# Optimization experiments

Hardware: AMD Instinct MI355X
Metric: run time of the kernel (lower is better)

The kernel has to match this reference:

```python
import jax, jax.numpy as jnp
import numpy as np

DIM = 96
GROUPS = 8          # SPPE factor
CG = DIM // GROUPS  # channels per SPPE group = 12
D_STATE = 16
D_CONV = 4
D_INNER = 2 * DIM   # expand=2
DT_RANK = 6         # ceil(96/16)
EPS = 1e-5


def setup_inputs() -> dict:
    key = jax.random.key(0)
    ks = jax.random.split(key, 16)
    def w(k, shape, s=0.02):
        return (jax.random.normal(k, shape) * s).astype(jnp.float32)
    z = lambda *s: jnp.zeros(s, jnp.float32)
    inp = {
        "x": jax.random.normal(ks[0], (2, DIM, 32, 32, 32), dtype=jnp.float32),
        # SPPE params
        "sppe_c1_w": w(ks[1], (CG, CG)), "sppe_c1_b": z(CG),
        "sppe_c3_w": w(ks[2], (CG, CG, 3, 3, 3)), "sppe_c3_b": z(CG),
        "sppe_gn_w": jnp.ones((CG,), jnp.float32), "sppe_gn_b": z(CG),
        # Mamba params (mamba_ssm defaults: proj biases False, conv bias True)
        "in_proj_w": w(ks[3], (2 * D_INNER, DIM)),
        "conv1d_w": w(ks[4], (D_INNER, D_CONV), 0.1), "conv1d_b": z(D_INNER),
        "x_proj_w": w(ks[5], (DT_RANK + 2 * D_STATE, D_INNER)),
        "dt_proj_w": w(ks[6], (D_INNER, DT_RANK), 0.1),
        "dt_proj_b": w(ks[7], (D_INNER,), 0.1),
        "A_log": jnp.log(jnp.tile(jnp.arange(1, D_STATE + 1, dtype=jnp.float32), (D_INNER, 1))),
        "ssm_D": jnp.ones((D_INNER,), jnp.float32),
        "out_proj_w": w(ks[8], (DIM, D_INNER)),
        # MlpChannel params (1x1 Conv3d == pointwise linear over channels)
        "mlp_fc1_w": w(ks[9], (4 * DIM, DIM)), "mlp_fc1_b": z(4 * DIM),
        "mlp_fc2_w": w(ks[10], (DIM, 4 * DIM)), "mlp_fc2_b": z(DIM),
    }
    return inp


def _inorm(x):
    # InstanceNorm3d (affine=False, biased var) over spatial dims per (b,c)
    m = jnp.mean(x, axis=(2, 3, 4), keepdims=True)
    v = jnp.var(x, axis=(2, 3, 4), keepdims=True)
    return (x - m) * jax.lax.rsqrt(v + EPS)


def _sppe(x, c1_w, c1_b, c3_w, c3_b, gn_w, gn_b):
    b, c, h, w, d = x.shape
    bg = b * GROUPS
    gx = x.reshape(bg, CG, h, w, d)
    # directional pools, each ending as (bg, CG, axis_len, 1, 1)
    x_h = jnp.mean(gx, axis=(3, 4), keepdims=True)                      # (bg,CG,h,1,1)
    x_w = jnp.mean(gx, axis=(2, 4), keepdims=True).transpose(0, 1, 3, 2, 4)
    x_d = jnp.mean(gx, axis=(2, 3), keepdims=True).transpose(0, 1, 4, 3, 2)
    hwd = jnp.concatenate([x_h, x_w, x_d], axis=2)[..., 0, 0]          # (bg,CG,h+w+d)
    hwd = jnp.einsum("oc,bcn->bon", c1_w, hwd) + c1_b[:, None]
    g_h = jax.nn.sigmoid(hwd[:, :, :h])[:, :, :, None, None]           # (bg,CG,h,1,1)
    g_w = jax.nn.sigmoid(hwd[:, :, h:h + w])[:, :, None, :, None]      # (bg,CG,1,w,1)
    g_d = jax.nn.sigmoid(hwd[:, :, h + w:])[:, :, None, None, :]       # (bg,CG,1,1,d)
    gated = gx * g_h * g_w * g_d
    # GroupNorm(num_groups=CG, num_channels=CG) == per-channel norm + affine
    gm = jnp.mean(gated, axis=(2, 3, 4), keepdims=True)
    gv = jnp.var(gated, axis=(2, 3, 4), keepdims=True)
    x1 = (gated - gm) * jax.lax.rsqrt(gv + EPS)
    x1 = x1 * gn_w[:, None, None, None] + gn_b[:, None, None, None]
    x2 = jax.lax.conv_general_dilated(
        gx, c3_w, (1, 1, 1), [(1, 1)] * 3,
        dimension_numbers=("NCDHW", "OIDHW", "NCDHW")) + c3_b[:, None, None, None]
    n = h * w * d
    x11 = jax.nn.softmax(jnp.mean(x1, axis=(2, 3, 4)), axis=-1)        # (bg,CG)
    x21 = jax.nn.softmax(jnp.mean(x2, axis=(2, 3, 4)), axis=-1)
    x12 = x2.reshape(bg, CG, n)
    x22 = x1.reshape(bg, CG, n)
    weights = (jnp.einsum("bc,bcn->bn", x11, x12)
               + jnp.einsum("bc,bcn->bn", x21, x22)).reshape(bg, 1, h, w, d)
    return (gx * jax.nn.sigmoid(weights)).reshape(b, c, h, w, d)


def _mamba(seq, in_proj_w, conv1d_w, conv1d_b, x_proj_w, dt_proj_w, dt_proj_b,
           A_log, ssm_D, out_proj_w):
    # seq: (B, L, DIM)
    B, L, _ = seq.shape
    xz = seq @ in_proj_w.T                       # (B,L,2*E)
    xm, zg = jnp.split(xz, 2, axis=-1)
    # depthwise causal conv1d along L
    xc = jax.lax.conv_general_dilated(
        xm.transpose(0, 2, 1), conv1d_w[:, None, :], (1,), [(D_CONV - 1, 0)],
        dimension_numbers=("NCH", "OIH", "NCH"), feature_group_count=D_INNER)
    xc = jax.nn.silu((xc + conv1d_b[:, None]).transpose(0, 2, 1))  # (B,L,E)
    dbl = xc @ x_proj_w.T                         # (B,L,DT_RANK+2N)
    dt = jax.nn.softplus(dbl[..., :DT_RANK] @ dt_proj_w.T + dt_proj_b)  # (B,L,E)
    Bm = dbl[..., DT_RANK:DT_RANK + D_STATE]      # (B,L,N)
    Cm = dbl[..., DT_RANK + D_STATE:]             # (B,L,N)
    A = -jnp.exp(A_log)                           # (E,N)

    def step(h, t):
        dt_t, b_t, c_t, x_t = t                   # (B,E),(B,N),(B,N),(B,E)
        dA = jnp.exp(dt_t[:, :, None] * A)        # (B,E,N)
        h = h * dA + (dt_t * x_t)[:, :, None] * b_t[:, None, :]
        return h, jnp.einsum("ben,bn->be", h, c_t)

    h0 = jnp.zeros((B, D_INNER, D_STATE), seq.dtype)
    _, ys = jax.lax.scan(step, h0, (dt.transpose(1, 0, 2), Bm.transpose(1, 0, 2),
                                    Cm.transpose(1, 0, 2), xc.transpose(1, 0, 2)))
    y = ys.transpose(1, 0, 2) + xc * ssm_D
    y = y * jax.nn.silu(zg)
    return y @ out_proj_w.T                       # (B,L,DIM)


def reference(x, sppe_c1_w, sppe_c1_b, sppe_c3_w, sppe_c3_b, sppe_gn_w, sppe_gn_b,
              in_proj_w, conv1d_w, conv1d_b, x_proj_w, dt_proj_w, dt_proj_b,
              A_log, ssm_D, out_proj_w, mlp_fc1_w, mlp_fc1_b, mlp_fc2_w, mlp_fc2_b):
    y_sppe = _sppe(x, sppe_c1_w, sppe_c1_b, sppe_c3_w, sppe_c3_b, sppe_gn_w, sppe_gn_b)
    B, C, H, W, Dd = x.shape
    L = H * W * Dd
    seq = _inorm(x).reshape(B, C, L).transpose(0, 2, 1)           # (B,L,C)
    out = _mamba(seq, in_proj_w, conv1d_w, conv1d_b, x_proj_w,
                 dt_proj_w, dt_proj_b, A_log, ssm_D, out_proj_w)
    xo = out.transpose(0, 2, 1).reshape(B, C, H, W, Dd)
    xo = _inorm(xo) * y_sppe
    t = jnp.einsum("oc,bchwd->bohwd", mlp_fc1_w, xo) + mlp_fc1_b[:, None, None, None]
    t = jax.nn.gelu(t, approximate=False)
    t = jnp.einsum("oc,bchwd->bohwd", mlp_fc2_w, t) + mlp_fc2_b[:, None, None, None]
    return t + x
```

## Files before the change

kernel.cpp:

```cpp
#include <hip/hip_runtime.h>
#include <math.h>

#define NSPA 32768
#define TCH 32
#define NCH 1024
#define EPS 1e-5f

#define ST_MEAN   0
#define ST_RSTD   192
#define ST_GM     384
#define ST_GRSTD  576
#define ST_X2SUM  768
#define ST_XH     1024
#define ST_XW     7168
#define ST_XD     13312
#define ST_GATE   19456
#define ST_MEAN2  38400
#define ST_RSTD2  38592
#define ST_WT     40960

__device__ __forceinline__ float sigmoidf_(float x){ return 1.f/(1.f+__expf(-x)); }
__device__ __forceinline__ float siluf_(float x){ return x/(1.f+__expf(-x)); }
__device__ __forceinline__ float geluf_(float x){ return 0.5f*x*(1.f+erff(x*0.70710678118654752f)); }
__device__ __forceinline__ float softplusf_(float x){ return fmaxf(x,0.f) + log1pf(__expf(-fabsf(x))); }

__global__ void k_prep(const float* __restrict__ c3w, const float* __restrict__ W1,
                       const float* __restrict__ W2, const float* __restrict__ Wip,
                       const float* __restrict__ xpw,
                       float* __restrict__ wt, float* __restrict__ W1t,
                       float* __restrict__ W2t, float* __restrict__ Wipt,
                       float* __restrict__ xpWt) {
  int idx = blockIdx.x*256 + threadIdx.x;
  if (idx < 3888) {
    int co = idx/324, r = idx%324;
    wt[r*12+co] = c3w[co*324+r];
  } else if (idx < 40752) {
    int i = idx-3888; int k = i/384, h = i%384;
    W1t[i] = W1[(size_t)h*96+k];
  } else if (idx < 77616) {
    int i = idx-40752; int k = i/96, o = i%96;
    W2t[i] = W2[(size_t)o*384+k];
  } else if (idx < 114480) {
    int i = idx-77616; int k = i/384, r = i%384;
    Wipt[i] = Wip[(size_t)r*96+k];
  } else if (idx < 123696) {
    int i = idx-114480; int e = i/48, o = i%48;
    float v = 0.f;
    if (o < 38) { int row = (o<32)? (o+6) : (o-32); v = xpw[(size_t)row*192+e]; }
    xpWt[i] = v;
  }
}

__global__ void k_stats(const float* __restrict__ x, float* __restrict__ st) {
  int bc = blockIdx.x;
  int t = threadIdx.x;
  __shared__ float xh_s[32], xw_s[32], xd_s[32], red[16], red2[16];
  if (t < 32) { xh_s[t]=0.f; xw_s[t]=0.f; xd_s[t]=0.f; }
  __syncthreads();
  const float* px = x + (size_t)bc*NSPA;
  float s=0.f, s2=0.f;
  for (int it=0; it<32; ++it) {
    float v = px[it*1024 + t];
    s += v; s2 += v*v;
    float wv = v;
    #pragma unroll
    for (int m=32;m>=1;m>>=1) wv += __shfl_xor(wv,m);
    if ((t&63)==0) atomicAdd(&xh_s[it], wv);
  }
  atomicAdd(&xw_s[(t>>5)&31], s);
  atomicAdd(&xd_s[t&31], s);
  float rs=s, rs2=s2;
  #pragma unroll
  for (int m=32;m>=1;m>>=1){ rs += __shfl_xor(rs,m); rs2 += __shfl_xor(rs2,m); }
  if ((t&63)==0){ red[t>>6]=rs; red2[t>>6]=rs2; }
  __syncthreads();
  if (t==0){
    float S=0.f,S2=0.f;
    for (int w=0;w<16;w++){ S+=red[w]; S2+=red2[w]; }
    float mn = S/(float)NSPA;
    float var = S2/(float)NSPA - mn*mn;
    st[ST_MEAN+bc] = mn;
    st[ST_RSTD+bc] = rsqrtf(var+EPS);
  }
  if (t<32){
    st[ST_XH + bc*32 + t] = xh_s[t]*(1.f/1024.f);
    st[ST_XW + bc*32 + t] = xw_s[t]*(1.f/1024.f);
    st[ST_XD + bc*32 + t] = xd_s[t]*(1.f/1024.f);
  }
}

__global__ void k_gates(const float* __restrict__ c1w, const float* __restrict__ c1b,
                        float* __restrict__ st) {
  int bg = blockIdx.x; int b = bg>>3; int g = bg&7;
  for (int i = threadIdx.x; i < 12*96; i += 128) {
    int co = i/96, pos = i%96;
    float acc = c1b[co];
    for (int cg=0; cg<12; ++cg) {
      int bc = b*96 + g*12 + cg;
      float hv;
      if (pos < 32)      hv = st[ST_XH + bc*32 + pos];
      else if (pos < 64) hv = st[ST_XW + bc*32 + pos-32];
      else               hv = st[ST_XD + bc*32 + pos-64];
      acc += c1w[co*12+cg]*hv;
    }
    st[ST_GATE + bg*1152 + i] = sigmoidf_(acc);
  }
}

__global__ void k_gated(const float* __restrict__ x, float* __restrict__ gated,
                        float* __restrict__ st) {
  int bc = blockIdx.x; int bg = bc/12; int cg = bc%12;
  int t = threadIdx.x;
  const float* gate = st + ST_GATE + bg*1152 + cg*96;
  float gw = gate[32 + (t>>5)];
  float gd = gate[64 + (t&31)];
  const float* px = x + (size_t)bc*NSPA;
  float* pg = gated + (size_t)bc*NSPA;
  __shared__ float red[16], red2[16];
  float s=0.f, s2=0.f;
  for (int it=0; it<32; ++it) {
    float gh = gate[it];
    float v = px[it*1024+t]*gh*gw*gd;
    pg[it*1024+t] = v;
    s += v; s2 += v*v;
  }
  #pragma unroll
  for (int m=32;m>=1;m>>=1){ s += __shfl_xor(s,m); s2 += __shfl_xor(s2,m); }
  if ((t&63)==0){ red[t>>6]=s; red2[t>>6]=s2; }
  __syncthreads();
  if (t==0){
    float S=0.f,S2=0.f;
    for (int w=0;w<16;w++){ S+=red[w]; S2+=red2[w]; }
    float mn = S/(float)NSPA;
    float var = S2/(float)NSPA - mn*mn;
    st[ST_GM+bc] = mn;
    st[ST_GRSTD+bc] = rsqrtf(var+EPS);
  }
}

__global__ void k_conv3(const float* __restrict__ x, const float* __restrict__ wt,
                        const float* __restrict__ c3b, float* __restrict__ x2,
                        float* __restrict__ st) {
  __shared__ float sl[3][12*324];
  __shared__ float ssum[12];
  int bg = blockIdx.z;
  int w0 = (blockIdx.x & 1)*16, d0 = (blockIdx.x >> 1)*16;
  int h0 = blockIdx.y*4;
  int tid = threadIdx.x;
  if (tid < 12) ssum[tid] = 0.f;

  const float* xb = x + (size_t)bg*12*NSPA;

  auto load_slab = [&](int hh, int s){
    for (int i=tid; i<3888; i+=256){
      int ci = i/324, r = i%324;
      int lw = r/18, ld = r%18;
      int gw = w0-1+lw, gd = d0-1+ld;
      float v = 0.f;
      if ((unsigned)hh<32u && (unsigned)gw<32u && (unsigned)gd<32u)
        v = xb[(size_t)ci*NSPA + hh*1024 + gw*32 + gd];
      sl[s][i] = v;
    }
  };

  load_slab(h0-1, ((h0-1)%3+3)%3);
  load_slab(h0,   h0%3);
  load_slab(h0+1, (h0+1)%3);
  __syncthreads();

  int w = tid>>4, d = tid&15;
  int base_wd = w*18 + d;
  float b0v=c3b[0],b1v=c3b[1],b2v=c3b[2],b3v=c3b[3],b4v=c3b[4],b5v=c3b[5],
        b6v=c3b[6],b7v=c3b[7],b8v=c3b[8],b9v=c3b[9],b10v=c3b[10],b11v=c3b[11];

  for (int it=0; it<4; ++it){
    int h = h0 + it;
    const float* sm1 = sl[((h-1)%3+3)%3];
    const float* s00 = sl[h%3];
    const float* sp1 = sl[(h+1)%3];
    float acc[12];
    acc[0]=b0v; acc[1]=b1v; acc[2]=b2v; acc[3]=b3v; acc[4]=b4v; acc[5]=b5v;
    acc[6]=b6v; acc[7]=b7v; acc[8]=b8v; acc[9]=b9v; acc[10]=b10v; acc[11]=b11v;
    for (int ci=0; ci<12; ++ci){
      const float* w_ci = wt + ci*324;
      #pragma unroll
      for (int kh=0;kh<3;kh++){
        const float* sp = (kh==0)? sm1 : ((kh==1)? s00 : sp1);
        const float* srow = sp + ci*324 + base_wd;
        #pragma unroll
        for (int kw=0;kw<3;kw++){
          #pragma unroll
          for (int kd=0;kd<3;kd++){
            float v = srow[kw*18 + kd];
            const float4* wp = (const float4*)(w_ci + (kh*9+kw*3+kd)*12);
            float4 wa = wp[0], wb = wp[1], wc = wp[2];
            acc[0]=fmaf(wa.x,v,acc[0]); acc[1]=fmaf(wa.y,v,acc[1]);
            acc[2]=fmaf(wa.z,v,acc[2]); acc[3]=fmaf(wa.w,v,acc[3]);
            acc[4]=fmaf(wb.x,v,acc[4]); acc[5]=fmaf(wb.y,v,acc[5]);
            acc[6]=fmaf(wb.z,v,acc[6]); acc[7]=fmaf(wb.w,v,acc[7]);
            acc[8]=fmaf(wc.x,v,acc[8]); acc[9]=fmaf(wc.y,v,acc[9]);
            acc[10]=fmaf(wc.z,v,acc[10]); acc[11]=fmaf(wc.w,v,acc[11]);
          }
        }
      }
    }
    int l = h*1024 + (w0+w)*32 + (d0+d);
    #pragma unroll
    for (int co=0;co<12;co++){
      float r = acc[co];
      x2[(size_t)(bg*12+co)*NSPA + l] = r;
      float rv = r;
      #pragma unroll
      for (int m=32;m>=1;m>>=1) rv += __shfl_xor(rv,m);
      if ((tid&63)==0) atomicAdd(&ssum[co], rv);
    }
    __syncthreads();
    if (it<3){
      load_slab(h+2, (h+2)%3);
      __syncthreads();
    }
  }
  if (tid<12) atomicAdd(&st[ST_X2SUM + bg*12 + tid], ssum[tid]);
}

__global__ void k_sppe_out(const float* __restrict__ gated,
                           const float* __restrict__ x2, const float* __restrict__ gnw,
                           const float* __restrict__ gnb, const float* __restrict__ st,
                           float* __restrict__ sigb) {
  int bg = blockIdx.y; int b = bg>>3; int g = bg&7;
  __shared__ float x11s[12], alphas[12], betasum_s;
  if (threadIdx.x==0){
    float m1=-1e30f, m2=-1e30f;
    float mu2[12];
    for (int cg=0;cg<12;cg++){
      int bc=b*96+g*12+cg;
      mu2[cg] = st[ST_X2SUM+bc]*(1.f/(float)NSPA);
      m1 = fmaxf(m1, gnb[cg]); m2 = fmaxf(m2, mu2[cg]);
    }
    float e1[12], e2[12]; float s1=0.f, s2=0.f;
    for (int cg=0;cg<12;cg++){ e1[cg]=expf(gnb[cg]-m1); s1+=e1[cg];
                               e2[cg]=expf(mu2[cg]-m2); s2+=e2[cg]; }
    float bs=0.f;
    for (int cg=0;cg<12;cg++){
      int bc=b*96+g*12+cg;
      float x11 = e1[cg]/s1;
      float x21 = e2[cg]/s2;
      x11s[cg]=x11;
      float gr = st[ST_GRSTD+bc], gm = st[ST_GM+bc];
      alphas[cg] = x21*gr*gnw[cg];
      bs += x21*(gnb[cg] - gm*gr*gnw[cg]);
    }
    betasum_s = bs;
  }
  __syncthreads();
  int l = blockIdx.x*256 + threadIdx.x;
  float wsum = betasum_s;
  int bc0 = b*96+g*12;
  for (int cg=0;cg<12;cg++){
    size_t off = (size_t)(bc0+cg)*NSPA + l;
    wsum += x11s[cg]*x2[off] + alphas[cg]*gated[off];
  }
  sigb[(size_t)bg*NSPA + l] = sigmoidf_(wsum);
}

__global__ void k_front(const float* __restrict__ x, const float* __restrict__ Wipt,
                        const float* __restrict__ cw, const float* __restrict__ cb,
                        const float* __restrict__ st,
                        float* __restrict__ xc_t, float* __restrict__ zg_t) {
  __shared__ float As[96*64];
  __shared__ float outS[48*65];
  __shared__ float haloS[3*192];
  __shared__ float xhS[3*96];
  int b = blockIdx.y; int l0 = blockIdx.x*64; int tid = threadIdx.x;
  const float* mean = st + ST_MEAN + b*96;
  const float* rstd = st + ST_RSTD + b*96;
  for (int i=tid;i<96*64;i+=256){
    int k=i>>6, l=i&63;
    As[i] = (x[((size_t)b*96+k)*NSPA + l0+l]-mean[k])*rstd[k];
  }
  for (int i=tid;i<288;i+=256){
    int j=i/96, k=i%96;
    int t = l0-3+j;
    xhS[i] = (t>=0) ? (x[((size_t)b*96+k)*NSPA + t]-mean[k])*rstd[k] : 0.f;
  }
  __syncthreads();
  for (int i=tid;i<576;i+=256){
    int j=i/192, e=i%192;
    const float* xh = xhS + j*96;
    float s = 0.f;
    for (int k=0;k<96;k++) s = fmaf(Wipt[(size_t)k*384 + e], xh[k], s);
    haloS[j*192+e] = s;
  }
  __syncthreads();
  int wv = __builtin_amdgcn_readfirstlane(tid>>6);
  int lane = tid&63;
  for (int p=0;p<8;++p){
    int r0 = p*48 + wv*12;
    float acc[12];
    #pragma unroll
    for (int j=0;j<12;j++) acc[j]=0.f;
    for (int k=0;k<96;k++){
      float a = As[k*64+lane];
      const float4* wp = (const float4*)&Wipt[(size_t)k*384 + r0];
      float4 w0=wp[0],w1=wp[1],w2=wp[2];
      acc[0]=fmaf(w0.x,a,acc[0]);  acc[1]=fmaf(w0.y,a,acc[1]);
      acc[2]=fmaf(w0.z,a,acc[2]);  acc[3]=fmaf(w0.w,a,acc[3]);
      acc[4]=fmaf(w1.x,a,acc[4]);  acc[5]=fmaf(w1.y,a,acc[5]);
      acc[6]=fmaf(w1.z,a,acc[6]);  acc[7]=fmaf(w1.w,a,acc[7]);
      acc[8]=fmaf(w2.x,a,acc[8]);  acc[9]=fmaf(w2.y,a,acc[9]);
      acc[10]=fmaf(w2.z,a,acc[10]); acc[11]=fmaf(w2.w,a,acc[11]);
    }
    if (p) __syncthreads();
    if (p < 4){
      #pragma unroll
      for (int j=0;j<12;j++){
        int e = r0 + j;
        float v = acc[j];
        float vm1 = __shfl_up(v,1);
        float vm2 = __shfl_up(v,2);
        float vm3 = __shfl_up(v,3);
        if (lane==0) vm1 = haloS[2*192+e];
        if (lane<=1) vm2 = haloS[(1+lane)*192+e];
        if (lane<=2) vm3 = haloS[(0+lane)*192+e];
        float4 w4 = *(const float4*)&cw[e*4];
        float r_ = cb[e] + w4.x*vm3 + w4.y*vm2 + w4.z*vm1 + w4.w*v;
        outS[(wv*12+j)*65 + lane] = siluf_(r_);
      }
    } else {
      #pragma unroll
      for (int j=0;j<12;j++) outS[(wv*12+j)*65 + lane] = acc[j];
    }
    __syncthreads();
    float* dst = (p<4) ? xc_t : zg_t;
    int e0 = (p<4) ? p*48 : (p-4)*48;
    for (int i=tid; i<64*12; i+=256){
      int l = i/12, q = i%12;
      float4 v;
      v.x = outS[(q*4+0)*65 + l];
      v.y = outS[(q*4+1)*65 + l];
      v.z = outS[(q*4+2)*65 + l];
      v.w = outS[(q*4+3)*65 + l];
      *(float4*)&dst[((size_t)b*NSPA + l0+l)*192 + e0 + q*4] = v;
    }
  }
}

__global__ void k_gemm_xp(const float* __restrict__ A, const float* __restrict__ xpWt,
                          float* __restrict__ dbl_t) {
  __shared__ float As[96*65];
  __shared__ float dblS[48*65];
  int b = blockIdx.y; int l0 = blockIdx.x*64; int tid = threadIdx.x;
  int wv = __builtin_amdgcn_readfirstlane(tid>>6);
  int lane = tid&63;
  int o0 = wv*12;
  float acc[12];
  #pragma unroll
  for (int j=0;j<12;j++) acc[j]=0.f;
  for (int h=0;h<2;++h){
    if (h) __syncthreads();
    for (int i=tid;i<64*24;i+=256){
      int l=i/24, q=i%24;
      float4 v = *(const float4*)&A[((size_t)b*NSPA + l0+l)*192 + h*96 + q*4];
      As[(q*4+0)*65+l]=v.x; As[(q*4+1)*65+l]=v.y;
      As[(q*4+2)*65+l]=v.z; As[(q*4+3)*65+l]=v.w;
    }
    __syncthreads();
    for (int k=0;k<96;k++){
      float a = As[k*65+lane];
      const float4* wp = (const float4*)&xpWt[(size_t)(h*96+k)*48 + o0];
      float4 w0=wp[0],w1=wp[1],w2=wp[2];
      acc[0]=fmaf(w0.x,a,acc[0]);  acc[1]=fmaf(w0.y,a,acc[1]);
      acc[2]=fmaf(w0.z,a,acc[2]);  acc[3]=fmaf(w0.w,a,acc[3]);
      acc[4]=fmaf(w1.x,a,acc[4]);  acc[5]=fmaf(w1.y,a,acc[5]);
      acc[6]=fmaf(w1.z,a,acc[6]);  acc[7]=fmaf(w1.w,a,acc[7]);
      acc[8]=fmaf(w2.x,a,acc[8]);  acc[9]=fmaf(w2.y,a,acc[9]);
      acc[10]=fmaf(w2.z,a,acc[10]); acc[11]=fmaf(w2.w,a,acc[11]);
    }
  }
  __syncthreads();
  #pragma unroll
  for (int j=0;j<12;j++) dblS[(o0+j)*65 + lane] = acc[j];
  __syncthreads();
  for (int i=tid;i<64*10;i+=256){
    int l=i/10, q=i%10;
    float4 v;
    v.x = dblS[(q*4+0)*65+l]; v.y = dblS[(q*4+1)*65+l];
    v.z = dblS[(q*4+2)*65+l]; v.w = dblS[(q*4+3)*65+l];
    *(float4*)&dbl_t[((size_t)b*NSPA + l0+l)*40 + q*4] = v;
  }
}

__global__ void k_gemm_out(const float* __restrict__ A, const float* __restrict__ W,
                           float* __restrict__ out) {
  __shared__ float As[192*64];
  int b = blockIdx.y; int l0 = blockIdx.x*64; int tid = threadIdx.x;
  for (int f=tid; f<48*64; f+=256){
    int l = f&63, kq = f>>6;
    float4 v = *(const float4*)&A[((size_t)b*NSPA + l0+l)*192 + kq*4];
    As[(kq*4+0)*64+l]=v.x; As[(kq*4+1)*64+l]=v.y;
    As[(kq*4+2)*64+l]=v.z; As[(kq*4+3)*64+l]=v.w;
  }
  __syncthreads();
  int l4=(tid&15)*4; int og=tid>>4;
  for (int o0=og*4; o0<96; o0+=64){
    float acc[16];
    #pragma unroll
    for (int i=0;i<16;i++) acc[i]=0.f;
    for (int k=0;k<192;k++){
      float4 a = *(const float4*)&As[k*64+l4];
      #pragma unroll
      for (int j=0;j<4;j++){
        float wv = W[(size_t)(o0+j)*192+k];
        acc[j*4+0]+=wv*a.x; acc[j*4+1]+=wv*a.y; acc[j*4+2]+=wv*a.z; acc[j*4+3]+=wv*a.w;
      }
    }
    #pragma unroll
    for (int j=0;j<4;j++){
      int o=o0+j;
      float4 r; r.x=acc[j*4+0]; r.y=acc[j*4+1]; r.z=acc[j*4+2]; r.w=acc[j*4+3];
      *(float4*)&out[((size_t)b*96+o)*NSPA + l0+l4] = r;
    }
  }
}

__global__ void k_scanA(const float* __restrict__ xc_t, const float* __restrict__ dbl_t,
                        const float* __restrict__ dtw, const float* __restrict__ dtb,
                        const float* __restrict__ A_log,
                        float* __restrict__ P, float* __restrict__ hend) {
  int b = blockIdx.y, ch = blockIdx.x; int e = threadIdx.x;
  float An[16];
  #pragma unroll
  for (int n=0;n<16;n++) An[n] = -__expf(A_log[e*16+n]);
  float wdt[6];
  #pragma unroll
  for (int j=0;j<6;j++) wdt[j]=dtw[e*6+j];
  float bdt = dtb[e];
  const float* drow = dbl_t + ((size_t)b*NSPA + (size_t)ch*TCH)*40;
  const float* xrow = xc_t + ((size_t)b*NSPA + (size_t)ch*TCH)*192 + e;
  float h[16], Pp[16];
  #pragma unroll
  for (int n=0;n<16;n++){ h[n]=0.f; Pp[n]=1.f; }
  for (int l=0;l<TCH;l++){
    const float* u = drow + l*40;
    float4 b0=*(const float4*)(u+0), b1=*(const float4*)(u+4),
           b2=*(const float4*)(u+8), b3=*(const float4*)(u+12);
    float4 d4=*(const float4*)(u+32);
    float2 d2=*(const float2*)(u+36);
    float x = xrow[(size_t)l*192];
    float pre = bdt + wdt[0]*d4.x + wdt[1]*d4.y + wdt[2]*d4.z
                    + wdt[3]*d4.w + wdt[4]*d2.x + wdt[5]*d2.y;
    float dte = softplusf_(pre);
    float dtx = dte*x;
    float Bv[16] = {b0.x,b0.y,b0.z,b0.w, b1.x,b1.y,b1.z,b1.w,
                    b2.x,b2.y,b2.z,b2.w, b3.x,b3.y,b3.z,b3.w};
    #pragma unroll
    for (int n=0;n<16;n++){
      float a = __expf(dte*An[n]);
      Pp[n] *= a;
      h[n] = h[n]*a + dtx*Bv[n];
    }
  }
  size_t o = (((size_t)b*NCH+ch)*192+e)*16;
  #pragma unroll
  for (int q=0;q<4;q++){
    float4 rp; rp.x=Pp[q*4+0]; rp.y=Pp[q*4+1]; rp.z=Pp[q*4+2]; rp.w=Pp[q*4+3];
    *(float4*)&P[o+q*4] = rp;
    float4 rh; rh.x=h[q*4+0]; rh.y=h[q*4+1]; rh.z=h[q*4+2]; rh.w=h[q*4+3];
    *(float4*)&hend[o+q*4] = rh;
  }
}

__global__ void k_scanB(const float* __restrict__ P, const float* __restrict__ hend,
                        float* __restrict__ Hs) {
  __shared__ float sP[16][64], sH[16][64];
  int b = blockIdx.y;
  int rl = threadIdx.x & 63;
  int cg = threadIdx.x >> 6;
  int r  = blockIdx.x*64 + rl;
  size_t base = (size_t)b*NCH*3072 + r;
  int c0 = cg*64;
  float Pl = 1.f, hl = 0.f;
  for (int c=c0; c<c0+64; ++c){
    size_t idx = base + (size_t)c*3072;
    float Pc = P[idx], Hc = hend[idx];
    hl = fmaf(Pc, hl, Hc);
    Pl *= Pc;
  }
  sP[cg][rl] = Pl; sH[cg][rl] = hl;
  __syncthreads();
  float H = 0.f;
  for (int g=0; g<cg; ++g) H = fmaf(sP[g][rl], H, sH[g][rl]);
  for (int c=c0; c<c0+64; ++c){
    size_t idx = base + (size_t)c*3072;
    float Pc = P[idx], Hc = hend[idx];
    Hs[idx] = H;
    H = fmaf(Pc, H, Hc);
  }
}

__global__ void k_scanC(const float* xc_t, const float* __restrict__ dbl_t,
                        const float* __restrict__ dtw, const float* __restrict__ dtb,
                        const float* __restrict__ A_log, const float* __restrict__ Hs,
                        const float* __restrict__ ssm_D, const float* __restrict__ zg_t,
                        float* y_t) {
  int b = blockIdx.y, ch = blockIdx.x; int e = threadIdx.x;
  float An[16];
  #pragma unroll
  for (int n=0;n<16;n++) An[n] = -__expf(A_log[e*16+n]);
  float wdt[6];
  #pragma unroll
  for (int j=0;j<6;j++) wdt[j]=dtw[e*6+j];
  float bdt = dtb[e];
  float Dv = ssm_D[e];
  const float* drow = dbl_t + ((size_t)b*NSPA + (size_t)ch*TCH)*40;
  const float* xrow = xc_t + ((size_t)b*NSPA + (size_t)ch*TCH)*192 + e;
  const float* zrow = zg_t + ((size_t)b*NSPA + (size_t)ch*TCH)*192 + e;
  float* yrow = y_t + ((size_t)b*NSPA + (size_t)ch*TCH)*192 + e;
  float h[16];
  size_t ho = (((size_t)b*NCH+ch)*192+e)*16;
  #pragma unroll
  for (int q=0;q<4;q++){
    float4 hv = *(const float4*)&Hs[ho+q*4];
    h[q*4+0]=hv.x; h[q*4+1]=hv.y; h[q*4+2]=hv.z; h[q*4+3]=hv.w;
  }
  for (int l=0;l<TCH;l++){
    const float* u = drow + l*40;
    float4 b0=*(const float4*)(u+0), b1=*(const float4*)(u+4),
           b2=*(const float4*)(u+8), b3=*(const float4*)(u+12);
    float4 c0=*(const float4*)(u+16), c1=*(const float4*)(u+20),
           c2=*(const float4*)(u+24), c3=*(const float4*)(u+28);
    float4 d4=*(const float4*)(u+32);
    float2 d2=*(const float2*)(u+36);
    float x = xrow[(size_t)l*192];
    float z = zrow[(size_t)l*192];
    float pre = bdt + wdt[0]*d4.x + wdt[1]*d4.y + wdt[2]*d4.z
                    + wdt[3]*d4.w + wdt[4]*d2.x + wdt[5]*d2.y;
    float dte = softplusf_(pre);
    float dtx = dte*x;
    float Bv[16] = {b0.x,b0.y,b0.z,b0.w, b1.x,b1.y,b1.z,b1.w,
                    b2.x,b2.y,b2.z,b2.w, b3.x,b3.y,b3.z,b3.w};
    float Cv[16] = {c0.x,c0.y,c0.z,c0.w, c1.x,c1.y,c1.z,c1.w,
                    c2.x,c2.y,c2.z,c2.w, c3.x,c3.y,c3.z,c3.w};
    float yp = 0.f;
    #pragma unroll
    for (int n=0;n<16;n++){
      float a = __expf(dte*An[n]);
      h[n] = h[n]*a + dtx*Bv[n];
      yp += h[n]*Cv[n];
    }
    yrow[(size_t)l*192] = (yp + x*Dv)*siluf_(z);
  }
}

__global__ void k_stats2(const float* __restrict__ outb, float* __restrict__ st) {
  int bc = blockIdx.x; int t = threadIdx.x;
  const float* p = outb + (size_t)bc*NSPA;
  float s=0.f, s2=0.f;
  for (int i=t;i<NSPA;i+=256){ float v=p[i]; s+=v; s2+=v*v; }
  __shared__ float red[4], red2[4];
  #pragma unroll
  for (int m=32;m>=1;m>>=1){ s += __shfl_xor(s,m); s2 += __shfl_xor(s2,m); }
  if ((t&63)==0){ red[t>>6]=s; red2[t>>6]=s2; }
  __syncthreads();
  if (t==0){
    float S=red[0]+red[1]+red[2]+red[3];
    float S2=red2[0]+red2[1]+red2[2]+red2[3];
    float mn=S/(float)NSPA; float var=S2/(float)NSPA-mn*mn;
    st[ST_MEAN2+bc]=mn; st[ST_RSTD2+bc]=rsqrtf(var+EPS);
  }
}

__global__ void k_mlpF(const float* __restrict__ outb, const float* __restrict__ sigb,
                       const float* __restrict__ st,
                       const float* __restrict__ W1t, const float* __restrict__ b1,
                       const float* __restrict__ W2t, const float* __restrict__ b2,
                       const float* __restrict__ x, float* __restrict__ dout) {
  __shared__ float xoS[96*64];
  __shared__ float hidS[64*64];
  int b = blockIdx.y; int l0 = blockIdx.x*64; int tid = threadIdx.x;
  for (int i=tid;i<96*64;i+=256){
    int k=i>>6, l=i&63;
    size_t off = ((size_t)b*96+k)*NSPA + l0+l;
    float sv = sigb[((size_t)(b*8 + k/12))*NSPA + l0+l];
    xoS[i] = (outb[off]-st[ST_MEAN2+b*96+k])*st[ST_RSTD2+b*96+k]*x[off]*sv;
  }
  __syncthreads();
  int wv = __builtin_amdgcn_readfirstlane(tid >> 6);
  int lane = tid & 63;
  float acc2[24];
  #pragma unroll
  for (int i=0;i<24;i++) acc2[i]=0.f;
  int o0 = wv*24;

  for (int c=0; c<6; ++c){
    int h0 = c*64 + wv*16;
    float acc1[16];
    #pragma unroll
    for (int i=0;i<16;i++) acc1[i]=0.f;
    for (int k=0;k<96;k++){
      float a = xoS[k*64 + lane];
      const float4* wp = (const float4*)&W1t[(size_t)k*384 + h0];
      float4 w0=wp[0], w1=wp[1], w2=wp[2], w3=wp[3];
      acc1[0]=fmaf(w0.x,a,acc1[0]);  acc1[1]=fmaf(w0.y,a,acc1[1]);
      acc1[2]=fmaf(w0.z,a,acc1[2]);  acc1[3]=fmaf(w0.w,a,acc1[3]);
      acc1[4]=fmaf(w1.x,a,acc1[4]);  acc1[5]=fmaf(w1.y,a,acc1[5]);
      acc1[6]=fmaf(w1.z,a,acc1[6]);  acc1[7]=fmaf(w1.w,a,acc1[7]);
      acc1[8]=fmaf(w2.x,a,acc1[8]);  acc1[9]=fmaf(w2.y,a,acc1[9]);
      acc1[10]=fmaf(w2.z,a,acc1[10]); acc1[11]=fmaf(w2.w,a,acc1[11]);
      acc1[12]=fmaf(w3.x,a,acc1[12]); acc1[13]=fmaf(w3.y,a,acc1[13]);
      acc1[14]=fmaf(w3.z,a,acc1[14]); acc1[15]=fmaf(w3.w,a,acc1[15]);
    }
    if (c) __syncthreads();
    #pragma unroll
    for (int j=0;j<16;j++)
      hidS[(wv*16+j)*64 + lane] = geluf_(acc1[j] + b1[h0+j]);
    __syncthreads();
    for (int k2=0;k2<64;k2++){
      float a = hidS[k2*64 + lane];
      int kg = c*64 + k2;
      const float4* wp = (const float4*)&W2t[(size_t)kg*96 + o0];
      float4 w0=wp[0], w1=wp[1], w2=wp[2], w3=wp[3], w4=wp[4], w5=wp[5];
      acc2[0]=fmaf(w0.x,a,acc2[0]);  acc2[1]=fmaf(w0.y,a,acc2[1]);
      acc2[2]=fmaf(w0.z,a,acc2[2]);  acc2[3]=fmaf(w0.w,a,acc2[3]);
      acc2[4]=fmaf(w1.x,a,acc2[4]);  acc2[5]=fmaf(w1.y,a,acc2[5]);
      acc2[6]=fmaf(w1.z,a,acc2[6]);  acc2[7]=fmaf(w1.w,a,acc2[7]);
      acc2[8]=fmaf(w2.x,a,acc2[8]);  acc2[9]=fmaf(w2.y,a,acc2[9]);
      acc2[10]=fmaf(w2.z,a,acc2[10]); acc2[11]=fmaf(w2.w,a,acc2[11]);
      acc2[12]=fmaf(w3.x,a,acc2[12]); acc2[13]=fmaf(w3.y,a,acc2[13]);
      acc2[14]=fmaf(w3.z,a,acc2[14]); acc2[15]=fmaf(w3.w,a,acc2[15]);
      acc2[16]=fmaf(w4.x,a,acc2[16]); acc2[17]=fmaf(w4.y,a,acc2[17]);
      acc2[18]=fmaf(w4.z,a,acc2[18]); acc2[19]=fmaf(w4.w,a,acc2[19]);
      acc2[20]=fmaf(w5.x,a,acc2[20]); acc2[21]=fmaf(w5.y,a,acc2[21]);
      acc2[22]=fmaf(w5.z,a,acc2[22]); acc2[23]=fmaf(w5.w,a,acc2[23]);
    }
  }
  #pragma unroll
  for (int j=0;j<24;j++){
    int o = o0 + j;
    size_t off = ((size_t)b*96+o)*NSPA + l0 + lane;
    dout[off] = acc2[j] + b2[o] + x[off];
  }
}

extern "C" void kernel_launch(void* const* d_in, const int* in_sizes, int n_in,
                              void* d_out, int out_size, void* d_ws, size_t ws_size,
                              hipStream_t stream) {
  const float* x        = (const float*)d_in[0];
  const float* c1w      = (const float*)d_in[1];
  const float* c1b      = (const float*)d_in[2];
  const float* c3w      = (const float*)d_in[3];
  const float* c3b      = (const float*)d_in[4];
  const float* gnw      = (const float*)d_in[5];
  const float* gnb      = (const float*)d_in[6];
  const float* in_proj  = (const float*)d_in[7];
  const float* conv1dw  = (const float*)d_in[8];
  const float* conv1db  = (const float*)d_in[9];
  const float* xprojw   = (const float*)d_in[10];
  const float* dtw      = (const float*)d_in[11];
  const float* dtb      = (const float*)d_in[12];
  const float* A_log    = (const float*)d_in[13];
  const float* ssm_D    = (const float*)d_in[14];
  const float* outprojw = (const float*)d_in[15];
  const float* W1       = (const float*)d_in[16];
  const float* b1       = (const float*)d_in[17];
  const float* W2       = (const float*)d_in[18];
  const float* b2       = (const float*)d_in[19];
  float* dout = (float*)d_out;

  float* ws = (float*)d_ws;
  const size_t o_st = 0;
  const size_t o_A  = 65536;
  const size_t o_B  = o_A + 12582912;
  const size_t o_C  = o_B + 12582912;
  const size_t o_D  = o_C + 12582912;
  const size_t o_E  = o_D + 6291456;
  const size_t o_F  = o_E + 6291456;
  float* st    = ws + o_st;
  float* P     = ws + o_A;
  float* Hs    = ws + o_A + 6291456;
  float* zg_t  = ws + o_B;
  float* xc_t  = ws + o_C;
  float* y_t   = ws + o_C;
  float* gated = ws + o_D;
  float* dbl_t = ws + o_D;
  float* x2b   = ws + o_E;
  float* hendb = ws + o_E;
  float* outb  = ws + o_E;
  float* W1t   = ws + o_F + 0;
  float* W2t   = ws + o_F + 40960;
  float* Wipt  = ws + o_F + 81920;
  float* xpWt  = ws + o_F + 122880;
  float* sigb  = ws + o_F + 200704;
  float* wtb   = st + ST_WT;

  hipMemsetAsync(st, 0, 65536*sizeof(float), stream);

  k_prep<<<484, 256, 0, stream>>>(c3w, W1, W2, in_proj, xprojw,
                                  wtb, W1t, W2t, Wipt, xpWt);
  k_stats<<<192, 1024, 0, stream>>>(x, st);
  k_gates<<<16, 128, 0, stream>>>(c1w, c1b, st);
  k_gated<<<192, 1024, 0, stream>>>(x, gated, st);
  k_conv3<<<dim3(4,8,16), 256, 0, stream>>>(x, wtb, c3b, x2b, st);
  k_sppe_out<<<dim3(128,16), 256, 0, stream>>>(gated, x2b, gnw, gnb, st, sigb);
  k_front<<<dim3(512,2), 256, 0, stream>>>(x, Wipt, conv1dw, conv1db,
                                           st, xc_t, zg_t);
  k_gemm_xp<<<dim3(512,2), 256, 0, stream>>>(xc_t, xpWt, dbl_t);
  k_scanA<<<dim3(NCH,2), 192, 0, stream>>>(xc_t, dbl_t, dtw, dtb, A_log, P, hendb);
  k_scanB<<<dim3(48,2), 1024, 0, stream>>>(P, hendb, Hs);
  k_scanC<<<dim3(NCH,2), 192, 0, stream>>>(xc_t, dbl_t, dtw, dtb, A_log, Hs,
                                           ssm_D, zg_t, y_t);
  k_gemm_out<<<dim3(512,2), 256, 0, stream>>>(y_t, outprojw, outb);
  k_stats2<<<192, 256, 0, stream>>>(outb, st);
  k_mlpF<<<dim3(512,2), 256, 0, stream>>>(outb, sigb, st, W1t, b1, W2t, b2, x, dout);
}
```

Baseline: 845.4 us.

## Fuse out-projection GEMM into the scan output kernel via shared memory

The separate out-projection GEMM kernel is removed. Each scanC block now stores its 32x192 gated y tile in shared memory and multiplies it by a transposed out_proj weight, prepared in k_prep, writing channel-major output directly. This avoids writing and re-reading the full y tensor in global memory and saves one launch. In exchange, scanC needs about 25KB of shared memory per block and an extra GEMM phase, which may lower occupancy, and its output stores are only 32 floats wide per row.

```diff
diff --git a/kernel.cpp b/kernel.cpp
--- a/kernel.cpp
+++ b/kernel.cpp
@@ -26,10 +26,10 @@
 
 __global__ void k_prep(const float* __restrict__ c3w, const float* __restrict__ W1,
                        const float* __restrict__ W2, const float* __restrict__ Wip,
-                       const float* __restrict__ xpw,
+                       const float* __restrict__ xpw, const float* __restrict__ Wout,
                        float* __restrict__ wt, float* __restrict__ W1t,
                        float* __restrict__ W2t, float* __restrict__ Wipt,
-                       float* __restrict__ xpWt) {
+                       float* __restrict__ xpWt, float* __restrict__ Wot) {
   int idx = blockIdx.x*256 + threadIdx.x;
   if (idx < 3888) {
     int co = idx/324, r = idx%324;
@@ -48,6 +48,9 @@
     float v = 0.f;
     if (o < 38) { int row = (o<32)? (o+6) : (o-32); v = xpw[(size_t)row*192+e]; }
     xpWt[i] = v;
+  } else if (idx < 142128) {
+    int i = idx-123696; int e = i/96, o = i%96;
+    Wot[i] = Wout[(size_t)o*192+e];
   }
 }
 
@@ -390,39 +393,6 @@
   }
 }
 
-__global__ void k_gemm_out(const float* __restrict__ A, const float* __restrict__ W,
-                           float* __restrict__ out) {
-  __shared__ float As[192*64];
-  int b = blockIdx.y; int l0 = blockIdx.x*64; int tid = threadIdx.x;
-  for (int f=tid; f<48*64; f+=256){
-    int l = f&63, kq = f>>6;
-    float4 v = *(const float4*)&A[((size_t)b*NSPA + l0+l)*192 + kq*4];
-    As[(kq*4+0)*64+l]=v.x; As[(kq*4+1)*64+l]=v.y;
-    As[(kq*4+2)*64+l]=v.z; As[(kq*4+3)*64+l]=v.w;
-  }
-  __syncthreads();
-  int l4=(tid&15)*4; int og=tid>>4;
-  for (int o0=og*4; o0<96; o0+=64){
-    float acc[16];
-    #pragma unroll
-    for (int i=0;i<16;i++) acc[i]=0.f;
-    for (int k=0;k<192;k++){
-      float4 a = *(const float4*)&As[k*64+l4];
-      #pragma unroll
-      for (int j=0;j<4;j++){
-        float wv = W[(size_t)(o0+j)*192+k];
-        acc[j*4+0]+=wv*a.x; acc[j*4+1]+=wv*a.y; acc[j*4+2]+=wv*a.z; acc[j*4+3]+=wv*a.w;
-      }
-    }
-    #pragma unroll
-    for (int j=0;j<4;j++){
-      int o=o0+j;
-      float4 r; r.x=acc[j*4+0]; r.y=acc[j*4+1]; r.z=acc[j*4+2]; r.w=acc[j*4+3];
-      *(float4*)&out[((size_t)b*96+o)*NSPA + l0+l4] = r;
-    }
-  }
-}
-
 __global__ void k_scanA(const float* __restrict__ xc_t, const float* __restrict__ dbl_t,
                         const float* __restrict__ dtw, const float* __restrict__ dtb,
                         const float* __restrict__ A_log,
@@ -498,11 +468,12 @@
   }
 }
 
-__global__ void k_scanC(const float* xc_t, const float* __restrict__ dbl_t,
+__global__ void k_scanC(const float* __restrict__ xc_t, const float* __restrict__ dbl_t,
                         const float* __restrict__ dtw, const float* __restrict__ dtb,
                         const float* __restrict__ A_log, const float* __restrict__ Hs,
                         const float* __restrict__ ssm_D, const float* __restrict__ zg_t,
-                        float* y_t) {
+                        const float* __restrict__ Wot, float* __restrict__ out) {
+  __shared__ float yS[32*193];
   int b = blockIdx.y, ch = blockIdx.x; int e = threadIdx.x;
   float An[16];
   #pragma unroll
@@ -515,7 +486,6 @@
   const float* drow = dbl_t + ((size_t)b*NSPA + (size_t)ch*TCH)*40;
   const float* xrow = xc_t + ((size_t)b*NSPA + (size_t)ch*TCH)*192 + e;
   const float* zrow = zg_t + ((size_t)b*NSPA + (size_t)ch*TCH)*192 + e;
-  float* yrow = y_t + ((size_t)b*NSPA + (size_t)ch*TCH)*192 + e;
   float h[16];
   size_t ho = (((size_t)b*NCH+ch)*192+e)*16;
   #pragma unroll
@@ -548,7 +518,33 @@
       h[n] = h[n]*a + dtx*Bv[n];
       yp += h[n]*Cv[n];
     }
-    yrow[(size_t)l*192] = (yp + x*Dv)*siluf_(z);
+    yS[l*193 + e] = (yp + x*Dv)*siluf_(z);
+  }
+  __syncthreads();
+  int tl = e & 31;
+  int og = e >> 5;
+  int o0 = og*16;
+  float acc[16];
+  #pragma unroll
+  for (int i=0;i<16;i++) acc[i]=0.f;
+  const float* yrowS = yS + tl*193;
+  for (int k=0;k<192;k++){
+    float a = yrowS[k];
+    const float4* wp = (const float4*)&Wot[(size_t)k*96 + o0];
+    float4 w0=wp[0], w1=wp[1], w2=wp[2], w3=wp[3];
+    acc[0]=fmaf(w0.x,a,acc[0]);  acc[1]=fmaf(w0.y,a,acc[1]);
+    acc[2]=fmaf(w0.z,a,acc[2]);  acc[3]=fmaf(w0.w,a,acc[3]);
+    acc[4]=fmaf(w1.x,a,acc[4]);  acc[5]=fmaf(w1.y,a,acc[5]);
+    acc[6]=fmaf(w1.z,a,acc[6]);  acc[7]=fmaf(w1.w,a,acc[7]);
+    acc[8]=fmaf(w2.x,a,acc[8]);  acc[9]=fmaf(w2.y,a,acc[9]);
+    acc[10]=fmaf(w2.z,a,acc[10]); acc[11]=fmaf(w2.w,a,acc[11]);
+    acc[12]=fmaf(w3.x,a,acc[12]); acc[13]=fmaf(w3.y,a,acc[13]);
+    acc[14]=fmaf(w3.z,a,acc[14]); acc[15]=fmaf(w3.w,a,acc[15]);
+  }
+  int lbase = ch*TCH + tl;
+  #pragma unroll
+  for (int j=0;j<16;j++){
+    out[((size_t)b*96 + o0+j)*NSPA + lbase] = acc[j];
   }
 }
 
@@ -680,7 +676,6 @@
   float* Hs    = ws + o_A + 6291456;
   float* zg_t  = ws + o_B;
   float* xc_t  = ws + o_C;
-  float* y_t   = ws + o_C;
   float* gated = ws + o_D;
   float* dbl_t = ws + o_D;
   float* x2b   = ws + o_E;
@@ -690,13 +685,14 @@
   float* W2t   = ws + o_F + 40960;
   float* Wipt  = ws + o_F + 81920;
   float* xpWt  = ws + o_F + 122880;
+  float* Wot   = ws + o_F + 139264;
   float* sigb  = ws + o_F + 200704;
   float* wtb   = st + ST_WT;
 
   hipMemsetAsync(st, 0, 65536*sizeof(float), stream);
 
-  k_prep<<<484, 256, 0, stream>>>(c3w, W1, W2, in_proj, xprojw,
-                                  wtb, W1t, W2t, Wipt, xpWt);
+  k_prep<<<556, 256, 0, stream>>>(c3w, W1, W2, in_proj, xprojw, outprojw,
+                                  wtb, W1t, W2t, Wipt, xpWt, Wot);
   k_stats<<<192, 1024, 0, stream>>>(x, st);
   k_gates<<<16, 128, 0, stream>>>(c1w, c1b, st);
   k_gated<<<192, 1024, 0, stream>>>(x, gated, st);
@@ -708,8 +704,7 @@
   k_scanA<<<dim3(NCH,2), 192, 0, stream>>>(xc_t, dbl_t, dtw, dtb, A_log, P, hendb);
   k_scanB<<<dim3(48,2), 1024, 0, stream>>>(P, hendb, Hs);
   k_scanC<<<dim3(NCH,2), 192, 0, stream>>>(xc_t, dbl_t, dtw, dtb, A_log, Hs,
-                                           ssm_D, zg_t, y_t);
-  k_gemm_out<<<dim3(512,2), 256, 0, stream>>>(y_t, outprojw, outb);
+                                           ssm_D, zg_t, Wot, outb);
   k_stats2<<<192, 256, 0, stream>>>(outb, st);
   k_mlpF<<<dim3(512,2), 256, 0, stream>>>(outb, sigb, st, W1t, b1, W2t, b2, x, dout);
 }
```

Result: no change. 845.5 us (+0.0%).
